# Kernel optimization log

Measured on AMD Instinct MI355X. Metric: run time of the kernel, lower is better.

## Reference

```python
import jax, jax.numpy as jnp
import numpy as np

EPS = 1e-12  # torch F.normalize eps

def _l2norm(v, axis):
    n = jnp.sqrt(jnp.sum(v * v, axis=axis, keepdims=True))
    return v / jnp.maximum(n, EPS)

def setup_inputs() -> dict:
    key = jax.random.key(0)
    k1, k2, k3 = jax.random.split(key, 3)
    B, M, D, K = 32, 2048, 1024, 64
    init_sc = 1.0 / np.sqrt(D)
    x = jax.random.normal(k1, (B, M, D), dtype=jnp.float32)
    W = init_sc * jax.random.normal(k2, (K, D), dtype=jnp.float32)          # fc1.weight
    centroids = init_sc * jax.random.normal(k3, (K, D), dtype=jnp.float32)  # self.centeroids
    return {"x": x, "W": W, "centroids": centroids}

def reference(x, W, centroids):
    # x: [B, M, D] frame features; W, centroids: [K, D]
    x = _l2norm(x, axis=-1)                                   # per-frame L2 normalize
    logits = jnp.einsum('bmd,kd->bmk', x, W)                  # fc1 (no bias)
    a = jax.nn.softmax(logits, axis=-1)                       # soft assignment [B, M, K]
    # vlad[b,k,:] = sum_m a[b,m,k] * (x[b,m,:] - centroids[k,:])
    #            = (A^T X)[b,k,:] - (sum_m a[b,m,k]) * centroids[k,:]
    vlad = jnp.einsum('bmk,bmd->bkd', a, x) - a.sum(axis=1)[..., None] * centroids
    vlad = _l2norm(vlad, axis=-1)                             # intra-normalization per cluster
    v = vlad.reshape(vlad.shape[0], -1)                       # [B, K*D]
    return _l2norm(v, axis=-1)                                # global L2 normalize
```

## Files before the change

kernel.cpp:

```cpp
#include <hip/hip_runtime.h>
#include <math.h>


#define NB 32
#define NM 2048
#define ND 1024
#define NK 64

typedef float f32x4 __attribute__((ext_vector_type(4)));
typedef short s16x4 __attribute__((ext_vector_type(4)));
typedef short s16x8 __attribute__((ext_vector_type(8)));

static constexpr float EPS_ = 1e-12f;

__device__ __forceinline__ short f2bf(float f) {
    union { float f; unsigned u; } v; v.f = f;
    unsigned r = v.u + 0x7fffu + ((v.u >> 16) & 1u);
    return (short)(r >> 16);
}
__device__ __forceinline__ int cvt2(float lo, float hi) {
    int r; asm("v_cvt_pk_bf16_f32 %0, %1, %2" : "=v"(r) : "v"(lo), "v"(hi));
    return r;
}
__device__ __forceinline__ int4 cvt8(const float4 a, const float4 b) {
    int4 r;
    r.x = cvt2(a.x, a.y); r.y = cvt2(a.z, a.w);
    r.z = cvt2(b.x, b.y); r.w = cvt2(b.z, b.w);
    return r;
}

__device__ __forceinline__ void gload16(const void* g, void* l) {
    __builtin_amdgcn_global_load_lds(
        (const __attribute__((address_space(1))) void*)g,
        (__attribute__((address_space(3))) void*)l, 16, 0, 0);
}

__global__ __launch_bounds__(256) void nv1_logits_softmax(
    const float* __restrict__ x, const float* __restrict__ W,
    short* __restrict__ aT, short* __restrict__ xbT, float* __restrict__ asum_part)
{
    const int b = blockIdx.y, mt = blockIdx.x;
    const int tid  = threadIdx.x;
    const int w    = tid >> 6, lane = tid & 63, g = lane >> 4, c = lane & 15;
    const int wm   = w >> 1, wk = w & 1;

    __shared__ union {
        struct { short Xs[64][72]; short Ws[64][72]; } st;
        float Ls[64][68];
    } sm;
    __shared__ float red[64][8];
    __shared__ float inv_l[64];
    __shared__ float asum_l[64];

    f32x4 acc[2][2] = {};
    float sq[2] = {0.f, 0.f};

    const int r0  = tid >> 3;
    const int dg8 = (tid & 7) << 3;
    const float* xb = x + ((size_t)b * NM + (size_t)mt * 64) * ND;
    const size_t tb = ((size_t)(b * 32 + mt) * 8) << 13;

    for (int d0 = 0; d0 < ND; d0 += 64) {
        __syncthreads();
        const int d    = d0 + dg8;
        const int dblk = (d >> 4) & 7;
        const size_t gpb = tb + ((size_t)(d >> 7) << 13) + (size_t)dblk * 1024 + (size_t)(d & 15);
        #pragma unroll
        for (int j = 0; j < 2; ++j) {
            const int r = r0 + 32 * j;
            const float4 xv0 = *(const float4*)(xb + (size_t)r * ND + d);
            const float4 xv1 = *(const float4*)(xb + (size_t)r * ND + d + 4);
            const float4 wv0 = *(const float4*)(W  + (size_t)r * ND + d);
            const float4 wv1 = *(const float4*)(W  + (size_t)r * ND + d + 4);
            sq[j] += xv0.x*xv0.x + xv0.y*xv0.y + xv0.z*xv0.z + xv0.w*xv0.w
                   + xv1.x*xv1.x + xv1.y*xv1.y + xv1.z*xv1.z + xv1.w*xv1.w;
            const int4 px = cvt8(xv0, xv1);
            const int4 pw = cvt8(wv0, wv1);
            *(int4*)&sm.st.Xs[r][dg8] = px;
            *(int4*)&sm.st.Ws[r][dg8] = pw;
            *(int4*)(xbT + gpb + (size_t)(r >> 2) * 64 + (size_t)(r & 3) * 16) = px;
        }
        __syncthreads();
        #pragma unroll
        for (int s = 0; s < 2; ++s) {
            s16x8 af[2], bf[2];
            #pragma unroll
            for (int f = 0; f < 2; ++f) {
                af[f] = *(const s16x8*)&sm.st.Xs[wm*32 + f*16 + c][s*32 + g*8];
                bf[f] = *(const s16x8*)&sm.st.Ws[wk*32 + f*16 + c][s*32 + g*8];
            }
            #pragma unroll
            for (int fm = 0; fm < 2; ++fm)
                #pragma unroll
                for (int fk = 0; fk < 2; ++fk)
                    acc[fm][fk] = __builtin_amdgcn_mfma_f32_16x16x32_bf16(
                        af[fm], bf[fk], acc[fm][fk], 0, 0, 0);
        }
    }
    __syncthreads();
    red[r0][tid & 7]      = sq[0];
    red[r0 + 32][tid & 7] = sq[1];
    #pragma unroll
    for (int fm = 0; fm < 2; ++fm)
        #pragma unroll
        for (int fk = 0; fk < 2; ++fk)
            #pragma unroll
            for (int r = 0; r < 4; ++r)
                sm.Ls[wm*32 + fm*16 + g*4 + r][wk*32 + fk*16 + c] = acc[fm][fk][r];
    __syncthreads();
    if (tid < 64) {
        float s = 0.f;
        #pragma unroll
        for (int i = 0; i < 8; ++i) s += red[tid][i];
        inv_l[tid]  = 1.f / fmaxf(sqrtf(s), EPS_);
        asum_l[tid] = 0.f;
    }
    __syncthreads();

    const int row = tid >> 2, q = tid & 3;
    const float iv = inv_l[row];
    float e[16];
    float mx = -3.0e38f;
    #pragma unroll
    for (int j = 0; j < 16; ++j) { e[j] = sm.Ls[row][q*16 + j] * iv; mx = fmaxf(mx, e[j]); }
    mx = fmaxf(mx, __shfl_xor(mx, 1, 64));
    mx = fmaxf(mx, __shfl_xor(mx, 2, 64));
    float smv = 0.f;
    #pragma unroll
    for (int j = 0; j < 16; ++j) { e[j] = __expf(e[j] - mx); smv += e[j]; }
    smv += __shfl_xor(smv, 1, 64);
    smv += __shfl_xor(smv, 2, 64);
    const float rs = 1.f / smv;
    #pragma unroll
    for (int j = 0; j < 16; ++j) e[j] *= rs;

    {
        int4 p0, p1;
        p0.x = cvt2(e[0]*iv,  e[1]*iv);  p0.y = cvt2(e[2]*iv,  e[3]*iv);
        p0.z = cvt2(e[4]*iv,  e[5]*iv);  p0.w = cvt2(e[6]*iv,  e[7]*iv);
        p1.x = cvt2(e[8]*iv,  e[9]*iv);  p1.y = cvt2(e[10]*iv, e[11]*iv);
        p1.z = cvt2(e[12]*iv, e[13]*iv); p1.w = cvt2(e[14]*iv, e[15]*iv);
        const size_t base = ((size_t)(b * 32 + mt)) * 4096
                          + (size_t)(q * 16 + (row >> 2)) * 64 + (size_t)(row & 3) * 16;
        *(int4*)(aT + base)     = p0;
        *(int4*)(aT + base + 8) = p1;
    }
    #pragma unroll
    for (int msk = 4; msk <= 32; msk <<= 1)
        #pragma unroll
        for (int j = 0; j < 16; ++j) e[j] += __shfl_xor(e[j], msk, 64);
    if ((tid & 60) == 0)
        #pragma unroll
        for (int j = 0; j < 16; ++j) atomicAdd(&asum_l[q*16 + j], e[j]);
    __syncthreads();
    if (tid < 64) asum_part[(size_t)(b * 32 + mt) * 64 + tid] = asum_l[tid];
}

__global__ __launch_bounds__(512) void nv2_vlad(
    const short* __restrict__ xbT, const short* __restrict__ aT,
    const float* __restrict__ asum_part, const float* __restrict__ cent,
    float* __restrict__ out, float* __restrict__ rowsq_part)
{
    const int b = blockIdx.y, dt = blockIdx.x;
    const int tid  = threadIdx.x;
    const int w    = tid >> 6, lane = tid & 63, g = lane >> 4, c = lane & 15;
    const int wk   = w >> 2, wd = w & 3;

    __shared__ short Xl[4][8192];
    __shared__ short Al[4][4096];
    __shared__ float rsq_l[64];
    __shared__ float asum_s[64];

    if (tid < 64) {
        rsq_l[tid] = 0.f;
        float s = 0.f;
        const float* ap = asum_part + (size_t)b * 2048 + tid;
        #pragma unroll
        for (int j = 0; j < 32; ++j) s += ap[j * 64];
        asum_s[tid] = s;
    }

    f32x4 acc[2][2] = {};

    auto STAGE = [&](int mc, int p) {
        const short* xs  = xbT + (((size_t)(b * 32 + mc) * 8 + dt) << 13);
        const short* as_ = aT  + ((size_t)(b * 32 + mc) << 12);
        gload16(xs  + w * 1024 + lane * 8,       &Xl[p][w * 1024]);
        gload16(xs  + w * 1024 + 512 + lane * 8, &Xl[p][w * 1024 + 512]);
        gload16(as_ + w * 512 + lane * 8,        &Al[p][w * 512]);
    };

    auto COMPUTE = [&](int p) {
        const uint32_t ab_ = (uint32_t)(uintptr_t)&Al[p][0];
        const uint32_t xb_ = (uint32_t)(uintptr_t)&Xl[p][0];
        s16x4 A[2][2][2], B[2][2][2];
        #pragma unroll
        for (int f = 0; f < 2; ++f)
            #pragma unroll
            for (int s = 0; s < 2; ++s)
                #pragma unroll
                for (int r = 0; r < 2; ++r) {
                    const uint32_t srow = (uint32_t)(s*8 + g*2 + r);
                    const uint32_t aoff = ab_ + (((uint32_t)(wk*2 + f)*16u + srow)*128u) + (uint32_t)c*8u;
                    const uint32_t boff = xb_ + (((uint32_t)(wd*2 + f)*16u + srow)*128u) + (uint32_t)c*8u;
                    asm volatile("ds_read_b64_tr_b16 %0, %1" : "=v"(A[f][s][r]) : "v"(aoff));
                    asm volatile("ds_read_b64_tr_b16 %0, %1" : "=v"(B[f][s][r]) : "v"(boff));
                }
        asm volatile("s_waitcnt lgkmcnt(0)" ::: "memory");
        __builtin_amdgcn_sched_barrier(0);
        #pragma unroll
        for (int s = 0; s < 2; ++s)
            #pragma unroll
            for (int fk = 0; fk < 2; ++fk) {
                const s16x8 af = __builtin_shufflevector(A[fk][s][0], A[fk][s][1], 0,1,2,3,4,5,6,7);
                #pragma unroll
                for (int fd = 0; fd < 2; ++fd) {
                    const s16x8 bf = __builtin_shufflevector(B[fd][s][0], B[fd][s][1], 0,1,2,3,4,5,6,7);
                    acc[fk][fd] = __builtin_amdgcn_mfma_f32_16x16x32_bf16(af, bf, acc[fk][fd], 0, 0, 0);
                }
            }
    };

    STAGE(0, 0);
    STAGE(1, 1);
    STAGE(2, 2);
    for (int mc = 0; mc < 32; ++mc) {
        if (mc < 30)      asm volatile("s_waitcnt vmcnt(6)" ::: "memory");
        else if (mc == 30) asm volatile("s_waitcnt vmcnt(3)" ::: "memory");
        else              asm volatile("s_waitcnt vmcnt(0)" ::: "memory");
        __builtin_amdgcn_s_barrier();
        if (mc + 3 < 32) STAGE(mc + 3, (mc + 3) & 3);
        COMPUTE(mc & 3);
    }

    const float* cb = cent + (size_t)dt * 128;
    #pragma unroll
    for (int fk = 0; fk < 2; ++fk)
        #pragma unroll
        for (int r = 0; r < 4; ++r) {
            const int k = wk*32 + fk*16 + g*4 + r;
            const float as = asum_s[k];
            float s2 = 0.f;
            #pragma unroll
            for (int fd = 0; fd < 2; ++fd) {
                const int d = wd*32 + fd*16 + c;
                const float v = acc[fk][fd][r] - as * cb[(size_t)k * ND + d];
                out[((size_t)b * 64 + k) * ND + (size_t)dt * 128 + d] = v;
                s2 += v * v;
            }
            s2 += __shfl_xor(s2, 1, 64);
            s2 += __shfl_xor(s2, 2, 64);
            s2 += __shfl_xor(s2, 4, 64);
            s2 += __shfl_xor(s2, 8, 64);
            if (c == 0) atomicAdd(&rsq_l[k], s2);
        }
    __syncthreads();
    if (tid < 64) rowsq_part[(size_t)(b * 8 + dt) * 64 + tid] = rsq_l[tid];
}

__global__ __launch_bounds__(256) void nv3_norm(
    float* __restrict__ out, const float* __restrict__ rowsq_part)
{
    const int b = blockIdx.y, ck = blockIdx.x;
    const int tid = threadIdx.x;
    __shared__ float rinv[64];
    __shared__ float gred[64];
    __shared__ float ginv_s;
    if (tid < 64) {
        float rs = 0.f;
        const float* rp = rowsq_part + (size_t)b * 512 + tid;
        #pragma unroll
        for (int j = 0; j < 8; ++j) rs += rp[j * 64];
        const float n = fmaxf(sqrtf(rs), EPS_);
        rinv[tid] = 1.f / n;
        gred[tid] = (rs / n) / n;
    }
    __syncthreads();
    if (tid == 0) {
        float s = 0.f;
        for (int k = 0; k < 64; ++k) s += gred[k];
        ginv_s = 1.f / fmaxf(sqrtf(s), EPS_);
    }
    __syncthreads();
    const float gi = ginv_s;
    float* ob = out + (size_t)b * (NK * ND);
    #pragma unroll
    for (int it = 0; it < 4; ++it) {
        const int idx = ck * 4096 + it * 1024 + tid * 4;
        const float sc = rinv[idx >> 10] * gi;
        float4 v = *(float4*)(ob + idx);
        v.x *= sc; v.y *= sc; v.z *= sc; v.w *= sc;
        *(float4*)(ob + idx) = v;
    }
}

extern "C" void kernel_launch(void* const* d_in, const int* in_sizes, int n_in,
                              void* d_out, int out_size, void* d_ws, size_t ws_size,
                              hipStream_t stream)
{
    const float* x    = (const float*)d_in[0];
    const float* W    = (const float*)d_in[1];
    const float* cent = (const float*)d_in[2];
    float* out = (float*)d_out;

    short* aT         = (short*)d_ws;
    short* xbT        = (short*)((char*)d_ws + (size_t)NB * NM * NK * 2);
    float* asum_part  = (float*)((char*)d_ws + (size_t)NB * NM * NK * 2 + (size_t)NB * NM * ND * 2);
    float* rowsq_part = asum_part + NB * 32 * 64;

    nv1_logits_softmax<<<dim3(NM / 64, NB), 256, 0, stream>>>(x, W, aT, xbT, asum_part);
    nv2_vlad<<<dim3(ND / 128, NB), 512, 0, stream>>>(xbT, aT, asum_part, cent, out, rowsq_part);
    nv3_norm<<<dim3(16, NB), 256, 0, stream>>>(out, rowsq_part);
}
```

Baseline: 428.8 us.

## Fuse logits/softmax with VLAD accumulation, keeping bf16 x tiles in LDS

Measured after the change: 427.4 us. No clear change (-0.3%).

```diff
diff --git a/kernel.cpp b/kernel.cpp
--- a/kernel.cpp
+++ b/kernel.cpp
@@ -13,11 +13,6 @@
 
 static constexpr float EPS_ = 1e-12f;
 
-__device__ __forceinline__ short f2bf(float f) {
-    union { float f; unsigned u; } v; v.f = f;
-    unsigned r = v.u + 0x7fffu + ((v.u >> 16) & 1u);
-    return (short)(r >> 16);
-}
 __device__ __forceinline__ int cvt2(float lo, float hi) {
     int r; asm("v_cvt_pk_bf16_f32 %0, %1, %2" : "=v"(r) : "v"(lo), "v"(hi));
     return r;
@@ -29,233 +24,217 @@
     return r;
 }
 
-__device__ __forceinline__ void gload16(const void* g, void* l) {
-    __builtin_amdgcn_global_load_lds(
-        (const __attribute__((address_space(1))) void*)g,
-        (__attribute__((address_space(3))) void*)l, 16, 0, 0);
-}
-
-__global__ __launch_bounds__(256) void nv1_logits_softmax(
+struct SMem {
+    short xk[65536];
+    union { short Ws[2][64][72]; float Ls[64][68]; } u;
+    short at[4096];
+    float red[64][8];
+    float inv_l[64];
+    float asum_l[64];
+};
+
+__global__ __launch_bounds__(512, 2) void nv_fused(
     const float* __restrict__ x, const float* __restrict__ W,
-    short* __restrict__ aT, short* __restrict__ xbT, float* __restrict__ asum_part)
-{
-    const int b = blockIdx.y, mt = blockIdx.x;
+    float* __restrict__ part, float* __restrict__ asum_part)
+{
+    __shared__ SMem sm;
+    const int b = blockIdx.y, pb = blockIdx.x;
     const int tid  = threadIdx.x;
     const int w    = tid >> 6, lane = tid & 63, g = lane >> 4, c = lane & 15;
-    const int wm   = w >> 1, wk = w & 1;
-
-    __shared__ union {
-        struct { short Xs[64][72]; short Ws[64][72]; } st;
-        float Ls[64][68];
-    } sm;
-    __shared__ float red[64][8];
-    __shared__ float inv_l[64];
-    __shared__ float asum_l[64];
-
-    f32x4 acc[2][2] = {};
-    float sq[2] = {0.f, 0.f};
-
-    const int r0  = tid >> 3;
-    const int dg8 = (tid & 7) << 3;
-    const float* xb = x + ((size_t)b * NM + (size_t)mt * 64) * ND;
-    const size_t tb = ((size_t)(b * 32 + mt) * 8) << 13;
-
-    for (int d0 = 0; d0 < ND; d0 += 64) {
-        __syncthreads();
-        const int d    = d0 + dg8;
-        const int dblk = (d >> 4) & 7;
-        const size_t gpb = tb + ((size_t)(d >> 7) << 13) + (size_t)dblk * 1024 + (size_t)(d & 15);
-        #pragma unroll
-        for (int j = 0; j < 2; ++j) {
-            const int r = r0 + 32 * j;
-            const float4 xv0 = *(const float4*)(xb + (size_t)r * ND + d);
-            const float4 xv1 = *(const float4*)(xb + (size_t)r * ND + d + 4);
-            const float4 wv0 = *(const float4*)(W  + (size_t)r * ND + d);
-            const float4 wv1 = *(const float4*)(W  + (size_t)r * ND + d + 4);
-            sq[j] += xv0.x*xv0.x + xv0.y*xv0.y + xv0.z*xv0.z + xv0.w*xv0.w
-                   + xv1.x*xv1.x + xv1.y*xv1.y + xv1.z*xv1.z + xv1.w*xv1.w;
+    const int wm   = w >> 2, wk = w & 3;
+    const int row  = tid >> 3, q = tid & 7;
+
+    if (tid < 64) sm.asum_l[tid] = 0.f;
+
+    f32x4 vacc[4][8] = {};
+
+    const uint32_t xkb = (uint32_t)(uintptr_t)&sm.xk[0];
+    const uint32_t atb = (uint32_t)(uintptr_t)&sm.at[0];
+
+    for (int mc = 0; mc < 4; ++mc) {
+        const size_t xrow = ((size_t)b * NM + (size_t)pb * 256 + mc * 64 + row) * ND;
+        f32x4 lacc[2] = {};
+        float sq = 0.f;
+
+        auto A_MFMA = [&](int tt) {
+            #pragma unroll
+            for (int s = 0; s < 2; ++s) {
+                const int dd   = tt * 64 + s * 32 + g * 8;
+                const int dtl  = dd >> 7, dblk = (dd >> 4) & 7, dlo = dd & 15;
+                const s16x8 bfr = *(const s16x8*)&sm.u.Ws[tt & 1][wk * 16 + c][s * 32 + g * 8];
+                #pragma unroll
+                for (int f = 0; f < 2; ++f) {
+                    const int m = wm * 32 + f * 16 + c;
+                    const s16x8 afr = *(const s16x8*)&sm.xk[dtl * 8192
+                        + (dblk * 16 + (m >> 2)) * 64 + (m & 3) * 16 + dlo];
+                    lacc[f] = __builtin_amdgcn_mfma_f32_16x16x32_bf16(afr, bfr, lacc[f], 0, 0, 0);
+                }
+            }
+        };
+
+        for (int t = 0; t < 16; ++t) {
+            const int d = t * 64 + q * 8;
+            const float4 xv0 = *(const float4*)(x + xrow + d);
+            const float4 xv1 = *(const float4*)(x + xrow + d + 4);
+            const float4 wv0 = *(const float4*)(W + (size_t)row * ND + d);
+            const float4 wv1 = *(const float4*)(W + (size_t)row * ND + d + 4);
+            if (t > 0) A_MFMA(t - 1);
+            sq += xv0.x*xv0.x + xv0.y*xv0.y + xv0.z*xv0.z + xv0.w*xv0.w
+                + xv1.x*xv1.x + xv1.y*xv1.y + xv1.z*xv1.z + xv1.w*xv1.w;
             const int4 px = cvt8(xv0, xv1);
             const int4 pw = cvt8(wv0, wv1);
-            *(int4*)&sm.st.Xs[r][dg8] = px;
-            *(int4*)&sm.st.Ws[r][dg8] = pw;
-            *(int4*)(xbT + gpb + (size_t)(r >> 2) * 64 + (size_t)(r & 3) * 16) = px;
-        }
-        __syncthreads();
+            const int dblk = (d >> 4) & 7;
+            *(int4*)&sm.xk[(d >> 7) * 8192 + (dblk * 16 + (row >> 2)) * 64
+                           + (row & 3) * 16 + (d & 15)] = px;
+            *(int4*)&sm.u.Ws[t & 1][row][q * 8] = pw;
+            __syncthreads();
+        }
+        A_MFMA(15);
+        sm.red[row][q] = sq;
+        __syncthreads();
+
+        #pragma unroll
+        for (int f = 0; f < 2; ++f)
+            #pragma unroll
+            for (int r = 0; r < 4; ++r)
+                sm.u.Ls[wm * 32 + f * 16 + g * 4 + r][wk * 16 + c] = lacc[f][r];
+        if (tid < 64) {
+            float s = 0.f;
+            #pragma unroll
+            for (int i = 0; i < 8; ++i) s += sm.red[tid][i];
+            sm.inv_l[tid] = 1.f / fmaxf(sqrtf(s), EPS_);
+        }
+        __syncthreads();
+
+        {
+            const float iv = sm.inv_l[row];
+            float e[8];
+            float mx = -3.0e38f;
+            #pragma unroll
+            for (int j = 0; j < 8; ++j) { e[j] = sm.u.Ls[row][q * 8 + j] * iv; mx = fmaxf(mx, e[j]); }
+            mx = fmaxf(mx, __shfl_xor(mx, 1, 64));
+            mx = fmaxf(mx, __shfl_xor(mx, 2, 64));
+            mx = fmaxf(mx, __shfl_xor(mx, 4, 64));
+            float sv = 0.f;
+            #pragma unroll
+            for (int j = 0; j < 8; ++j) { e[j] = __expf(e[j] - mx); sv += e[j]; }
+            sv += __shfl_xor(sv, 1, 64);
+            sv += __shfl_xor(sv, 2, 64);
+            sv += __shfl_xor(sv, 4, 64);
+            const float rs = 1.f / sv;
+            #pragma unroll
+            for (int j = 0; j < 8; ++j) e[j] *= rs;
+            int4 av;
+            av.x = cvt2(e[0]*iv, e[1]*iv); av.y = cvt2(e[2]*iv, e[3]*iv);
+            av.z = cvt2(e[4]*iv, e[5]*iv); av.w = cvt2(e[6]*iv, e[7]*iv);
+            *(int4*)&sm.at[((q >> 1) * 16 + (row >> 2)) * 64 + (row & 3) * 16 + (q & 1) * 8] = av;
+            #pragma unroll
+            for (int j = 0; j < 8; ++j) {
+                e[j] += __shfl_xor(e[j], 8, 64);
+                e[j] += __shfl_xor(e[j], 16, 64);
+                e[j] += __shfl_xor(e[j], 32, 64);
+            }
+            if ((lane >> 3) == 0)
+                #pragma unroll
+                for (int j = 0; j < 8; ++j) atomicAdd(&sm.asum_l[q * 8 + j], e[j]);
+        }
+        __syncthreads();
+
         #pragma unroll
         for (int s = 0; s < 2; ++s) {
-            s16x8 af[2], bf[2];
-            #pragma unroll
-            for (int f = 0; f < 2; ++f) {
-                af[f] = *(const s16x8*)&sm.st.Xs[wm*32 + f*16 + c][s*32 + g*8];
-                bf[f] = *(const s16x8*)&sm.st.Ws[wk*32 + f*16 + c][s*32 + g*8];
+            s16x4 A[4][2], Bf[8][2];
+            #pragma unroll
+            for (int kf = 0; kf < 4; ++kf)
+                #pragma unroll
+                for (int r = 0; r < 2; ++r) {
+                    const uint32_t srow = (uint32_t)(s * 8 + g * 2 + r);
+                    const uint32_t aoff = atb + ((uint32_t)kf * 16u + srow) * 128u + (uint32_t)c * 8u;
+                    asm volatile("ds_read_b64_tr_b16 %0, %1" : "=v"(A[kf][r]) : "v"(aoff));
+                }
+            #pragma unroll
+            for (int fd = 0; fd < 8; ++fd)
+                #pragma unroll
+                for (int r = 0; r < 2; ++r) {
+                    const uint32_t srow = (uint32_t)(s * 8 + g * 2 + r);
+                    const uint32_t boff = xkb + (uint32_t)w * 16384u
+                                        + ((uint32_t)fd * 16u + srow) * 128u + (uint32_t)c * 8u;
+                    asm volatile("ds_read_b64_tr_b16 %0, %1" : "=v"(Bf[fd][r]) : "v"(boff));
+                }
+            asm volatile("s_waitcnt lgkmcnt(0)" ::: "memory");
+            __builtin_amdgcn_sched_barrier(0);
+            #pragma unroll
+            for (int kf = 0; kf < 4; ++kf) {
+                const s16x8 af = __builtin_shufflevector(A[kf][0], A[kf][1], 0,1,2,3,4,5,6,7);
+                #pragma unroll
+                for (int fd = 0; fd < 8; ++fd) {
+                    const s16x8 bf = __builtin_shufflevector(Bf[fd][0], Bf[fd][1], 0,1,2,3,4,5,6,7);
+                    vacc[kf][fd] = __builtin_amdgcn_mfma_f32_16x16x32_bf16(af, bf, vacc[kf][fd], 0, 0, 0);
+                }
             }
-            #pragma unroll
-            for (int fm = 0; fm < 2; ++fm)
-                #pragma unroll
-                for (int fk = 0; fk < 2; ++fk)
-                    acc[fm][fk] = __builtin_amdgcn_mfma_f32_16x16x32_bf16(
-                        af[fm], bf[fk], acc[fm][fk], 0, 0, 0);
-        }
-    }
-    __syncthreads();
-    red[r0][tid & 7]      = sq[0];
-    red[r0 + 32][tid & 7] = sq[1];
-    #pragma unroll
-    for (int fm = 0; fm < 2; ++fm)
-        #pragma unroll
-        for (int fk = 0; fk < 2; ++fk)
-            #pragma unroll
-            for (int r = 0; r < 4; ++r)
-                sm.Ls[wm*32 + fm*16 + g*4 + r][wk*32 + fk*16 + c] = acc[fm][fk][r];
-    __syncthreads();
+        }
+        __syncthreads();
+    }
+
+    float* pbase = part + (((size_t)(b * 8 + pb)) << 16);
+    #pragma unroll
+    for (int kf = 0; kf < 4; ++kf)
+        #pragma unroll
+        for (int r = 0; r < 4; ++r) {
+            const int k = kf * 16 + g * 4 + r;
+            #pragma unroll
+            for (int fd = 0; fd < 8; ++fd)
+                pbase[(size_t)k * ND + w * 128 + fd * 16 + c] = vacc[kf][fd][r];
+        }
+    if (tid < 64) asum_part[(b * 8 + pb) * 64 + tid] = sm.asum_l[tid];
+}
+
+__global__ __launch_bounds__(256) void nv_reduce(
+    const float* __restrict__ part, const float* __restrict__ asum_part,
+    const float* __restrict__ cent, float* __restrict__ out, float* __restrict__ rowsq_part)
+{
+    const int b = blockIdx.y, dt = blockIdx.x;
+    const int tid = threadIdx.x;
+    __shared__ float asum_s[64];
     if (tid < 64) {
         float s = 0.f;
         #pragma unroll
-        for (int i = 0; i < 8; ++i) s += red[tid][i];
-        inv_l[tid]  = 1.f / fmaxf(sqrtf(s), EPS_);
-        asum_l[tid] = 0.f;
+        for (int pbi = 0; pbi < 8; ++pbi) s += asum_part[(b * 8 + pbi) * 64 + tid];
+        asum_s[tid] = s;
     }
     __syncthreads();
-
-    const int row = tid >> 2, q = tid & 3;
-    const float iv = inv_l[row];
-    float e[16];
-    float mx = -3.0e38f;
-    #pragma unroll
-    for (int j = 0; j < 16; ++j) { e[j] = sm.Ls[row][q*16 + j] * iv; mx = fmaxf(mx, e[j]); }
-    mx = fmaxf(mx, __shfl_xor(mx, 1, 64));
-    mx = fmaxf(mx, __shfl_xor(mx, 2, 64));
-    float smv = 0.f;
-    #pragma unroll
-    for (int j = 0; j < 16; ++j) { e[j] = __expf(e[j] - mx); smv += e[j]; }
-    smv += __shfl_xor(smv, 1, 64);
-    smv += __shfl_xor(smv, 2, 64);
-    const float rs = 1.f / smv;
-    #pragma unroll
-    for (int j = 0; j < 16; ++j) e[j] *= rs;
-
-    {
-        int4 p0, p1;
-        p0.x = cvt2(e[0]*iv,  e[1]*iv);  p0.y = cvt2(e[2]*iv,  e[3]*iv);
-        p0.z = cvt2(e[4]*iv,  e[5]*iv);  p0.w = cvt2(e[6]*iv,  e[7]*iv);
-        p1.x = cvt2(e[8]*iv,  e[9]*iv);  p1.y = cvt2(e[10]*iv, e[11]*iv);
-        p1.z = cvt2(e[12]*iv, e[13]*iv); p1.w = cvt2(e[14]*iv, e[15]*iv);
-        const size_t base = ((size_t)(b * 32 + mt)) * 4096
-                          + (size_t)(q * 16 + (row >> 2)) * 64 + (size_t)(row & 3) * 16;
-        *(int4*)(aT + base)     = p0;
-        *(int4*)(aT + base + 8) = p1;
-    }
-    #pragma unroll
-    for (int msk = 4; msk <= 32; msk <<= 1)
-        #pragma unroll
-        for (int j = 0; j < 16; ++j) e[j] += __shfl_xor(e[j], msk, 64);
-    if ((tid & 60) == 0)
-        #pragma unroll
-        for (int j = 0; j < 16; ++j) atomicAdd(&asum_l[q*16 + j], e[j]);
-    __syncthreads();
-    if (tid < 64) asum_part[(size_t)(b * 32 + mt) * 64 + tid] = asum_l[tid];
-}
-
-__global__ __launch_bounds__(512) void nv2_vlad(
-    const short* __restrict__ xbT, const short* __restrict__ aT,
-    const float* __restrict__ asum_part, const float* __restrict__ cent,
-    float* __restrict__ out, float* __restrict__ rowsq_part)
-{
-    const int b = blockIdx.y, dt = blockIdx.x;
-    const int tid  = threadIdx.x;
-    const int w    = tid >> 6, lane = tid & 63, g = lane >> 4, c = lane & 15;
-    const int wk   = w >> 2, wd = w & 3;
-
-    __shared__ short Xl[4][8192];
-    __shared__ short Al[4][4096];
-    __shared__ float rsq_l[64];
-    __shared__ float asum_s[64];
-
-    if (tid < 64) {
-        rsq_l[tid] = 0.f;
-        float s = 0.f;
-        const float* ap = asum_part + (size_t)b * 2048 + tid;
-        #pragma unroll
-        for (int j = 0; j < 32; ++j) s += ap[j * 64];
-        asum_s[tid] = s;
-    }
-
-    f32x4 acc[2][2] = {};
-
-    auto STAGE = [&](int mc, int p) {
-        const short* xs  = xbT + (((size_t)(b * 32 + mc) * 8 + dt) << 13);
-        const short* as_ = aT  + ((size_t)(b * 32 + mc) << 12);
-        gload16(xs  + w * 1024 + lane * 8,       &Xl[p][w * 1024]);
-        gload16(xs  + w * 1024 + 512 + lane * 8, &Xl[p][w * 1024 + 512]);
-        gload16(as_ + w * 512 + lane * 8,        &Al[p][w * 512]);
-    };
-
-    auto COMPUTE = [&](int p) {
-        const uint32_t ab_ = (uint32_t)(uintptr_t)&Al[p][0];
-        const uint32_t xb_ = (uint32_t)(uintptr_t)&Xl[p][0];
-        s16x4 A[2][2][2], B[2][2][2];
-        #pragma unroll
-        for (int f = 0; f < 2; ++f)
-            #pragma unroll
-            for (int s = 0; s < 2; ++s)
-                #pragma unroll
-                for (int r = 0; r < 2; ++r) {
-                    const uint32_t srow = (uint32_t)(s*8 + g*2 + r);
-                    const uint32_t aoff = ab_ + (((uint32_t)(wk*2 + f)*16u + srow)*128u) + (uint32_t)c*8u;
-                    const uint32_t boff = xb_ + (((uint32_t)(wd*2 + f)*16u + srow)*128u) + (uint32_t)c*8u;
-                    asm volatile("ds_read_b64_tr_b16 %0, %1" : "=v"(A[f][s][r]) : "v"(aoff));
-                    asm volatile("ds_read_b64_tr_b16 %0, %1" : "=v"(B[f][s][r]) : "v"(boff));
-                }
-        asm volatile("s_waitcnt lgkmcnt(0)" ::: "memory");
-        __builtin_amdgcn_sched_barrier(0);
-        #pragma unroll
-        for (int s = 0; s < 2; ++s)
-            #pragma unroll
-            for (int fk = 0; fk < 2; ++fk) {
-                const s16x8 af = __builtin_shufflevector(A[fk][s][0], A[fk][s][1], 0,1,2,3,4,5,6,7);
-                #pragma unroll
-                for (int fd = 0; fd < 2; ++fd) {
-                    const s16x8 bf = __builtin_shufflevector(B[fd][s][0], B[fd][s][1], 0,1,2,3,4,5,6,7);
-                    acc[fk][fd] = __builtin_amdgcn_mfma_f32_16x16x32_bf16(af, bf, acc[fk][fd], 0, 0, 0);
-                }
-            }
-    };
-
-    STAGE(0, 0);
-    STAGE(1, 1);
-    STAGE(2, 2);
-    for (int mc = 0; mc < 32; ++mc) {
-        if (mc < 30)      asm volatile("s_waitcnt vmcnt(6)" ::: "memory");
-        else if (mc == 30) asm volatile("s_waitcnt vmcnt(3)" ::: "memory");
-        else              asm volatile("s_waitcnt vmcnt(0)" ::: "memory");
-        __builtin_amdgcn_s_barrier();
-        if (mc + 3 < 32) STAGE(mc + 3, (mc + 3) & 3);
-        COMPUTE(mc & 3);
-    }
-
-    const float* cb = cent + (size_t)dt * 128;
-    #pragma unroll
-    for (int fk = 0; fk < 2; ++fk)
-        #pragma unroll
-        for (int r = 0; r < 4; ++r) {
-            const int k = wk*32 + fk*16 + g*4 + r;
-            const float as = asum_s[k];
-            float s2 = 0.f;
-            #pragma unroll
-            for (int fd = 0; fd < 2; ++fd) {
-                const int d = wd*32 + fd*16 + c;
-                const float v = acc[fk][fd][r] - as * cb[(size_t)k * ND + d];
-                out[((size_t)b * 64 + k) * ND + (size_t)dt * 128 + d] = v;
-                s2 += v * v;
-            }
-            s2 += __shfl_xor(s2, 1, 64);
-            s2 += __shfl_xor(s2, 2, 64);
-            s2 += __shfl_xor(s2, 4, 64);
-            s2 += __shfl_xor(s2, 8, 64);
-            if (c == 0) atomicAdd(&rsq_l[k], s2);
-        }
-    __syncthreads();
-    if (tid < 64) rowsq_part[(size_t)(b * 8 + dt) * 64 + tid] = rsq_l[tid];
+    const int dq = (tid & 31) * 4;
+    const int kb = (tid >> 5) * 8;
+    float s2[8];
+    #pragma unroll
+    for (int kk = 0; kk < 8; ++kk) {
+        const int k = kb + kk;
+        float4 acc = make_float4(0.f, 0.f, 0.f, 0.f);
+        #pragma unroll
+        for (int pbi = 0; pbi < 8; ++pbi) {
+            const float4 p = *(const float4*)(part + (((size_t)(b * 8 + pbi)) << 16)
+                                              + (size_t)k * ND + dt * 128 + dq);
+            acc.x += p.x; acc.y += p.y; acc.z += p.z; acc.w += p.w;
+        }
+        const float as = asum_s[k];
+        const float4 cv = *(const float4*)(cent + (size_t)k * ND + dt * 128 + dq);
+        float4 v;
+        v.x = acc.x - as * cv.x; v.y = acc.y - as * cv.y;
+        v.z = acc.z - as * cv.z; v.w = acc.w - as * cv.w;
+        *(float4*)(out + ((size_t)b * NK + k) * ND + dt * 128 + dq) = v;
+        s2[kk] = v.x*v.x + v.y*v.y + v.z*v.z + v.w*v.w;
+    }
+    #pragma unroll
+    for (int kk = 0; kk < 8; ++kk) {
+        s2[kk] += __shfl_xor(s2[kk], 1, 64);
+        s2[kk] += __shfl_xor(s2[kk], 2, 64);
+        s2[kk] += __shfl_xor(s2[kk], 4, 64);
+        s2[kk] += __shfl_xor(s2[kk], 8, 64);
+        s2[kk] += __shfl_xor(s2[kk], 16, 64);
+    }
+    if ((tid & 31) == 0)
+        #pragma unroll
+        for (int kk = 0; kk < 8; ++kk)
+            rowsq_part[(b * 8 + dt) * 64 + kb + kk] = s2[kk];
 }
 
 __global__ __launch_bounds__(256) void nv3_norm(
@@ -303,12 +282,11 @@
     const float* cent = (const float*)d_in[2];
     float* out = (float*)d_out;
 
-    short* aT         = (short*)d_ws;
-    short* xbT        = (short*)((char*)d_ws + (size_t)NB * NM * NK * 2);
-    float* asum_part  = (float*)((char*)d_ws + (size_t)NB * NM * NK * 2 + (size_t)NB * NM * ND * 2);
-    float* rowsq_part = asum_part + NB * 32 * 64;
-
-    nv1_logits_softmax<<<dim3(NM / 64, NB), 256, 0, stream>>>(x, W, aT, xbT, asum_part);
-    nv2_vlad<<<dim3(ND / 128, NB), 512, 0, stream>>>(xbT, aT, asum_part, cent, out, rowsq_part);
+    float* part       = (float*)d_ws;
+    float* asum_part  = (float*)((char*)d_ws + ((size_t)256 << 18));
+    float* rowsq_part = asum_part + 256 * 64;
+
+    nv_fused<<<dim3(8, NB), 512, 0, stream>>>(x, W, part, asum_part);
+    nv_reduce<<<dim3(8, NB), 256, 0, stream>>>(part, asum_part, cent, out, rowsq_part);
     nv3_norm<<<dim3(16, NB), 256, 0, stream>>>(out, rowsq_part);
 }
```
